# Kernel optimization log

Hardware: AMD Instinct MI355X
Metric: run time of the kernel (lower is better)

## Reference

```python
import jax, jax.numpy as jnp
import numpy as np

DEPTH, DIM, DFF, VOCAB = 4, 512, 2048, 4096
EPS = 1e-5

def layernorm(x, w, b):
    mu = jnp.mean(x, axis=-1, keepdims=True)
    var = jnp.mean((x - mu) ** 2, axis=-1, keepdims=True)
    return (x - mu) * jax.lax.rsqrt(var + EPS) * w + b

def sconv(x, phazor_c, last_conv_c):
    # x: [B,L,dim] real; phazor_c, last_conv_c: [dim] complex
    B, L, D = x.shape
    r = jnp.abs(phazor_c)
    p = jnp.tanh(r) * jnp.exp(1j * jnp.angle(phazor_c))          # [dim]
    prog = p[None, :] ** jnp.arange(L, dtype=jnp.float32)[:, None]  # [L,dim]
    filt_fft = jnp.fft.fft(prog, n=2 * L, axis=0)                # [2L,dim]
    x_fft = jnp.fft.fft(x.astype(jnp.complex64), n=2 * L, axis=1)  # [B,2L,dim]
    conv = jnp.fft.ifft(filt_fft[None] * x_fft, axis=1)[:, :L]   # [B,L,dim]
    conv = conv + last_conv_c[None, None, :] * prog[None] * p[None, None, :]
    return conv.real.astype(x.dtype)

def setup_inputs() -> dict:
    key = jax.random.key(0)
    ks = jax.random.split(key, 20)
    f32 = jnp.float32
    inp = {}
    inp['x'] = jax.random.normal(ks[0], (2, 4096, VOCAB), dtype=f32)
    inp['Win'] = jax.random.normal(ks[1], (DIM, VOCAB), dtype=f32) * VOCAB ** -0.5
    inp['bin'] = jnp.zeros((DIM,), f32)
    inp['ln1_w'] = jnp.ones((DEPTH, DIM), f32)
    inp['ln1_b'] = jnp.zeros((DEPTH, DIM), f32)
    # phazor init: exp(2*pi*i*arange/dim)*|randn|
    ang = 2 * np.pi * jnp.arange(DIM, dtype=f32) / DIM
    mag = jnp.abs(jax.random.normal(ks[2], (DEPTH, DIM), dtype=f32))
    inp['phz_re'] = mag * jnp.cos(ang)[None]
    inp['phz_im'] = mag * jnp.sin(ang)[None]
    inp['lc_re'] = jax.random.normal(ks[3], (DEPTH, DIM), dtype=f32)
    inp['lc_im'] = jax.random.normal(ks[4], (DEPTH, DIM), dtype=f32)
    inp['sc_lin'] = jnp.ones((DEPTH, DIM), f32)
    inp['ln2_w'] = jnp.ones((DEPTH, DIM), f32)
    inp['ln2_b'] = jnp.zeros((DEPTH, DIM), f32)
    inp['W1'] = jax.random.normal(ks[5], (DEPTH, DFF, DIM), dtype=f32) * DIM ** -0.5
    inp['b1'] = jnp.zeros((DEPTH, DFF), f32)
    inp['W2'] = jax.random.normal(ks[6], (DEPTH, DIM, DFF), dtype=f32) * DFF ** -0.5
    inp['b2'] = jnp.zeros((DEPTH, DIM), f32)
    inp['lnl_w'] = jnp.ones((DIM,), f32)
    inp['lnl_b'] = jnp.zeros((DIM,), f32)
    inp['Wout'] = jax.random.normal(ks[7], (VOCAB, DIM), dtype=f32) * DIM ** -0.5
    inp['bout'] = jnp.zeros((VOCAB,), f32)
    return inp

def _forward(x, Win, bin, ln1_w, ln1_b, phz_re, phz_im, lc_re, lc_im, sc_lin,
             ln2_w, ln2_b, W1, b1, W2, b2, lnl_w, lnl_b, Wout, bout):
    h = jnp.einsum('blv,dv->bld', x, Win) + bin  # token_in

    def body(h, p):
        l1w, l1b, pr, pi, lr, li, scl, l2w, l2b, w1, b1_, w2, b2_ = p
        y = jax.nn.silu(layernorm(h, l1w, l1b))
        y = sconv(y, pr + 1j * pi, lr + 1j * li)
        h = h + y * scl
        y = layernorm(h, l2w, l2b)
        y = jax.nn.silu(jnp.einsum('bld,fd->blf', y, w1) + b1_)
        y = jnp.einsum('blf,df->bld', y, w2) + b2_
        return h + y, None

    xs = (ln1_w, ln1_b, phz_re, phz_im, lc_re, lc_im, sc_lin,
          ln2_w, ln2_b, W1, b1, W2, b2)
    h, _ = jax.lax.scan(body, h, xs)
    h = layernorm(h, lnl_w, lnl_b)
    return jnp.einsum('bld,vd->blv', h, Wout) + bout

def reference(x, Win, bin, ln1_w, ln1_b, phz_re, phz_im, lc_re, lc_im, sc_lin,
              ln2_w, ln2_b, W1, b1, W2, b2, lnl_w, lnl_b, Wout, bout):
    return _forward(x, Win, bin, ln1_w, ln1_b, phz_re, phz_im, lc_re, lc_im,
                    sc_lin, ln2_w, ln2_b, W1, b1, W2, b2, lnl_w, lnl_b, Wout, bout)
```

## Files before the change

### kernel.cpp

```cpp
#include <hip/hip_runtime.h>
#include <hip/hip_bf16.h>
#include <cstdint>
#include <cstddef>

#define DEPTH 4
#define DIM 512
#define DFF 2048
#define VOCAB 4096
#define NB 2
#define LSEQ 4096
#define MR (NB*LSEQ)
#define EPSL 1e-5f
#define NC 256
#define TCH 16

typedef __attribute__((ext_vector_type(8))) short  s8v;
typedef __attribute__((ext_vector_type(4))) float  f4v;
typedef __attribute__((ext_vector_type(8))) __bf16 bf8v;

__device__ __forceinline__ unsigned short f2b(float f) {
  union { float f; unsigned int u; } v; v.f = f;
  unsigned int r = v.u + 0x7FFFu + ((v.u >> 16) & 1u);
  return (unsigned short)(r >> 16);
}
__device__ __forceinline__ float b2f(unsigned short u) {
  union { unsigned int u; float f; } v; v.u = ((unsigned int)u) << 16; return v.f;
}

__device__ __forceinline__ void gld16(const void* g, void* l) {
  __builtin_amdgcn_global_load_lds(
      (const __attribute__((address_space(1))) unsigned int*)(uintptr_t)g,
      (__attribute__((address_space(3))) unsigned int*)(uintptr_t)l,
      16, 0, 0);
}

template<int N> __device__ __forceinline__ void wvm() {
  if constexpr (N == 8)      asm volatile("s_waitcnt vmcnt(8)" ::: "memory");
  else if constexpr (N == 6) asm volatile("s_waitcnt vmcnt(6)" ::: "memory");
  else if constexpr (N == 4) asm volatile("s_waitcnt vmcnt(4)" ::: "memory");
  else if constexpr (N == 3) asm volatile("s_waitcnt vmcnt(3)" ::: "memory");
  else                       asm volatile("s_waitcnt vmcnt(0)" ::: "memory");
}

__device__ __forceinline__ void wred64(float& s, float& s2) {
#pragma unroll
  for (int off = 32; off; off >>= 1) { s += __shfl_xor(s, off, 64); s2 += __shfl_xor(s2, off, 64); }
}

#define NX8 4194304
#define NW8  262144
#define N18  524288
#define N28  524288
#define NO8  262144
__global__ void __launch_bounds__(256) cvt_all(
    const float* __restrict__ x,  const float* __restrict__ Win,
    const float* __restrict__ W1, const float* __restrict__ W2,
    const float* __restrict__ Wout,
    unsigned short* __restrict__ xb,  unsigned short* __restrict__ Winb,
    unsigned short* __restrict__ W1b, unsigned short* __restrict__ W2b,
    unsigned short* __restrict__ Woutb)
{
  long i = (long)blockIdx.x * 256 + threadIdx.x;
  const float* src; unsigned short* dst; long j;
  if (i < NX8)                         { src = x;    dst = xb;    j = i; }
  else if (i < NX8 + NW8)              { src = Win;  dst = Winb;  j = i - NX8; }
  else if (i < NX8 + NW8 + N18)        { src = W1;   dst = W1b;   j = i - NX8 - NW8; }
  else if (i < NX8 + NW8 + N18 + N28)  { src = W2;   dst = W2b;   j = i - NX8 - NW8 - N18; }
  else                                 { src = Wout; dst = Woutb; j = i - NX8 - NW8 - N18 - N28; }
  const f4v* p = (const f4v*)(src + j * 8);
  f4v a = p[0], b = p[1];
  s8v o;
  o[0]=(short)f2b(a[0]); o[1]=(short)f2b(a[1]); o[2]=(short)f2b(a[2]); o[3]=(short)f2b(a[3]);
  o[4]=(short)f2b(b[0]); o[5]=(short)f2b(b[1]); o[6]=(short)f2b(b[2]); o[7]=(short)f2b(b[3]);
  *(s8v*)(dst + j * 8) = o;
}

__device__ __forceinline__ void phz2p(float re, float im, float& pre, float& pim) {
  float r = sqrtf(re * re + im * im);
  float t = (r > 1e-20f) ? (tanhf(r) / r) : 1.0f;
  pre = t * re; pim = t * im;
}

__device__ __forceinline__ void ln_silu_emit(
    float (*ls)[DIM], unsigned short* __restrict__ y,
    const float* __restrict__ lnw, const float* __restrict__ lnb,
    int wave, int c8, int b, int c)
{
  f4v w0 = *(const f4v*)(lnw + c8), w1 = *(const f4v*)(lnw + c8 + 4);
  f4v b0 = *(const f4v*)(lnb + c8), b1 = *(const f4v*)(lnb + c8 + 4);
#pragma unroll
  for (int jj = 0; jj < 2; ++jj) {
    int j = wave * 2 + jj;
    f4v v0 = *(const f4v*)&ls[j][c8];
    f4v v1 = *(const f4v*)&ls[j][c8 + 4];
    float s = 0.f, s2 = 0.f;
#pragma unroll
    for (int q = 0; q < 4; ++q) { s += v0[q]; s2 += v0[q]*v0[q]; s += v1[q]; s2 += v1[q]*v1[q]; }
    wred64(s, s2);
    float mu = s * (1.f / DIM);
    float rs = rsqrtf(s2 * (1.f / DIM) - mu * mu + EPSL);
    s8v ob;
    f4v o0, o1;
#pragma unroll
    for (int q = 0; q < 4; ++q) {
      float a = (v0[q] - mu) * rs * w0[q] + b0[q];
      a = a / (1.f + __expf(-a));
      unsigned short ua = f2b(a);
      ob[q] = (short)ua; o0[q] = b2f(ua);
      float e = (v1[q] - mu) * rs * w1[q] + b1[q];
      e = e / (1.f + __expf(-e));
      unsigned short ue = f2b(e);
      ob[4 + q] = (short)ue; o1[q] = b2f(ue);
    }
    *(s8v*)(y + ((size_t)b * LSEQ + (size_t)c * TCH + j) * DIM + c8) = ob;
    *(f4v*)&ls[j][c8]     = o0;
    *(f4v*)&ls[j][c8 + 4] = o1;
  }
}

__global__ void __launch_bounds__(512) red_ln_scan(
    const float* __restrict__ parts, float* __restrict__ h, const float* __restrict__ bias,
    const float* __restrict__ lnw, const float* __restrict__ lnb,
    const float* __restrict__ pr, const float* __restrict__ pi,
    unsigned short* __restrict__ y, float* __restrict__ stA)
{
  __shared__ float ls[TCH][DIM];
  const int d = threadIdx.x;
  const int c = blockIdx.x, b = blockIdx.y;
  const size_t rbase = ((size_t)b * LSEQ + (size_t)c * TCH) * DIM + d;
  const size_t st = (size_t)MR * DIM;
  const float bv = bias[d];
#pragma unroll 4
  for (int j = 0; j < TCH; ++j) {
    size_t o = rbase + (size_t)j * DIM;
    float v = parts[o] + parts[st + o] + bv;
    h[o] = v;
    ls[j][d] = v;
  }
  __syncthreads();
  const int wave = threadIdx.x >> 6, lane = threadIdx.x & 63;
  ln_silu_emit(ls, y, lnw, lnb, wave, lane * 8, b, c);
  __syncthreads();
  float pre, pim; phz2p(pr[d], pi[d], pre, pim);
  float sre = 0.f, sim = 0.f;
#pragma unroll
  for (int j = 0; j < TCH; ++j) {
    float xv = ls[j][d];
    float nre = fmaf(pre, sre, fmaf(-pim, sim, xv));
    float nim = fmaf(pre, sim, pim * sre);
    sre = nre; sim = nim;
  }
  size_t o = (((size_t)b * NC + c) * DIM + d) * 2;
  stA[o] = sre; stA[o + 1] = sim;
}

__global__ void __launch_bounds__(512) ln_scan(
    const float* __restrict__ h,
    const float* __restrict__ lnw, const float* __restrict__ lnb,
    const float* __restrict__ pr, const float* __restrict__ pi,
    unsigned short* __restrict__ y, float* __restrict__ stA)
{
  __shared__ float ls[TCH][DIM];
  const int d = threadIdx.x;
  const int c = blockIdx.x, b = blockIdx.y;
  const size_t rbase = ((size_t)b * LSEQ + (size_t)c * TCH) * DIM + d;
#pragma unroll 4
  for (int j = 0; j < TCH; ++j) ls[j][d] = h[rbase + (size_t)j * DIM];
  __syncthreads();
  const int wave = threadIdx.x >> 6, lane = threadIdx.x & 63;
  ln_silu_emit(ls, y, lnw, lnb, wave, lane * 8, b, c);
  __syncthreads();
  float pre, pim; phz2p(pr[d], pi[d], pre, pim);
  float sre = 0.f, sim = 0.f;
#pragma unroll
  for (int j = 0; j < TCH; ++j) {
    float xv = ls[j][d];
    float nre = fmaf(pre, sre, fmaf(-pim, sim, xv));
    float nim = fmaf(pre, sim, pim * sre);
    sre = nre; sim = nim;
  }
  size_t o = (((size_t)b * NC + c) * DIM + d) * 2;
  stA[o] = sre; stA[o + 1] = sim;
}

__global__ void __launch_bounds__(256) scan_b(
    const float* __restrict__ stA, float* __restrict__ carry,
    const float* __restrict__ pr, const float* __restrict__ pi,
    const float* __restrict__ lcr, const float* __restrict__ lci)
{
  int idx = blockIdx.x * 256 + threadIdx.x;
  int b = idx >> 9, d = idx & (DIM - 1);
  float pre, pim; phz2p(pr[d], pi[d], pre, pim);
  float qre = pre, qim = pim;
#pragma unroll
  for (int t = 0; t < 4; ++t) { float nr = qre*qre - qim*qim; float ni = 2.f*qre*qim; qre = nr; qim = ni; }
  float cre = lcr[d], cim = lci[d];
  const size_t base = (size_t)b * NC * DIM * 2 + (size_t)d * 2;
  for (int c0 = 0; c0 < NC; c0 += 8) {
    float ar[8], ai[8];
#pragma unroll
    for (int k = 0; k < 8; ++k) {
      size_t o = base + (size_t)(c0 + k) * DIM * 2;
      ar[k] = stA[o]; ai[k] = stA[o + 1];
    }
#pragma unroll
    for (int k = 0; k < 8; ++k) {
      size_t o = base + (size_t)(c0 + k) * DIM * 2;
      carry[o] = cre; carry[o + 1] = cim;
      float nr = fmaf(qre, cre, fmaf(-qim, cim, ar[k]));
      float ni = fmaf(qre, cim, fmaf(qim, cre, ai[k]));
      cre = nr; cim = ni;
    }
  }
}

__global__ void __launch_bounds__(512) scan_c_ln2(
    const unsigned short* __restrict__ y, float* __restrict__ h, const float* __restrict__ carry,
    const float* __restrict__ pr, const float* __restrict__ pi,
    const float* __restrict__ scl,
    const float* __restrict__ lnw, const float* __restrict__ lnb,
    unsigned short* __restrict__ yb)
{
  __shared__ float ls[TCH][DIM];
  const int d = threadIdx.x;
  const int c = blockIdx.x, b = blockIdx.y;
  float pre, pim; phz2p(pr[d], pi[d], pre, pim);
  size_t co = (((size_t)b * NC + c) * DIM + d) * 2;
  float sre = carry[co], sim = carry[co + 1];
  const float sc = scl[d];
  const size_t rbase = ((size_t)b * LSEQ + (size_t)c * TCH) * DIM + d;
#pragma unroll 4
  for (int j = 0; j < TCH; ++j) {
    size_t o = rbase + (size_t)j * DIM;
    float xv = b2f(y[o]);
    float nre = fmaf(pre, sre, fmaf(-pim, sim, xv));
    float nim = fmaf(pre, sim, pim * sre);
    sre = nre; sim = nim;
    float hv = h[o] + sre * sc;
    h[o] = hv;
    ls[j][d] = hv;
  }
  __syncthreads();
  const int wave = threadIdx.x >> 6, lane = threadIdx.x & 63;
  const int c8 = lane * 8;
  f4v w0 = *(const f4v*)(lnw + c8), w1 = *(const f4v*)(lnw + c8 + 4);
  f4v b0 = *(const f4v*)(lnb + c8), b1 = *(const f4v*)(lnb + c8 + 4);
#pragma unroll
  for (int jj = 0; jj < 2; ++jj) {
    int j = wave * 2 + jj;
    f4v v0 = *(const f4v*)&ls[j][c8];
    f4v v1 = *(const f4v*)&ls[j][c8 + 4];
    float s = 0.f, s2 = 0.f;
#pragma unroll
    for (int q = 0; q < 4; ++q) { s += v0[q]; s2 += v0[q]*v0[q]; s += v1[q]; s2 += v1[q]*v1[q]; }
    wred64(s, s2);
    float mu = s * (1.f / DIM);
    float rs = rsqrtf(s2 * (1.f / DIM) - mu * mu + EPSL);
    s8v o;
#pragma unroll
    for (int q = 0; q < 4; ++q) {
      o[q]     = (short)f2b((v0[q] - mu) * rs * w0[q] + b0[q]);
      o[4 + q] = (short)f2b((v1[q] - mu) * rs * w1[q] + b1[q]);
    }
    *(s8v*)(yb + ((size_t)b * LSEQ + (size_t)c * TCH + j) * DIM + c8) = o;
  }
}

__global__ void __launch_bounds__(512) ln_final(
    const float* __restrict__ h,
    const float* __restrict__ lnw, const float* __restrict__ lnb,
    unsigned short* __restrict__ yb)
{
  __shared__ float ls[TCH][DIM];
  const int d = threadIdx.x;
  const int c = blockIdx.x, b = blockIdx.y;
  const size_t rbase = ((size_t)b * LSEQ + (size_t)c * TCH) * DIM + d;
#pragma unroll 4
  for (int j = 0; j < TCH; ++j) ls[j][d] = h[rbase + (size_t)j * DIM];
  __syncthreads();
  const int wave = threadIdx.x >> 6, lane = threadIdx.x & 63;
  const int c8 = lane * 8;
  f4v w0 = *(const f4v*)(lnw + c8), w1 = *(const f4v*)(lnw + c8 + 4);
  f4v b0 = *(const f4v*)(lnb + c8), b1 = *(const f4v*)(lnb + c8 + 4);
#pragma unroll
  for (int jj = 0; jj < 2; ++jj) {
    int j = wave * 2 + jj;
    f4v v0 = *(const f4v*)&ls[j][c8];
    f4v v1 = *(const f4v*)&ls[j][c8 + 4];
    float s = 0.f, s2 = 0.f;
#pragma unroll
    for (int q = 0; q < 4; ++q) { s += v0[q]; s2 += v0[q]*v0[q]; s += v1[q]; s2 += v1[q]*v1[q]; }
    wred64(s, s2);
    float mu = s * (1.f / DIM);
    float rs = rsqrtf(s2 * (1.f / DIM) - mu * mu + EPSL);
    s8v o;
#pragma unroll
    for (int q = 0; q < 4; ++q) {
      o[q]     = (short)f2b((v0[q] - mu) * rs * w0[q] + b0[q]);
      o[4 + q] = (short)f2b((v1[q] - mu) * rs * w1[q] + b1[q]);
    }
    *(s8v*)(yb + ((size_t)b * LSEQ + (size_t)c * TCH + j) * DIM + c8) = o;
  }
}

template<int EPI, int BN>
__global__ void __launch_bounds__(256, BN == 64 ? 4 : 3) gemm_p(
    const unsigned short* __restrict__ A, const unsigned short* __restrict__ Bm,
    const float* __restrict__ bias,
    float* __restrict__ Cf, unsigned short* __restrict__ Cb,
    int N, int Keff, int lda, int ldb)
{
  constexpr int WN  = BN / 2;
  constexpr int NJ  = WN / 16;
  constexpr int VPT = 2 + BN / 64;
  __shared__ unsigned short As[3][128 * 32];
  __shared__ unsigned short Bs[3][BN * 32];
  const int tid  = threadIdx.x;
  const int lane = tid & 63, wave = tid >> 6;
  const int wm = wave >> 1, wn = wave & 1;
  const int fr = lane & 15, fq = lane >> 4;
  const int bz = blockIdx.z;

  int bx, by;
  {
    int gx = gridDim.x;
    int nwg = gx * gridDim.y;
    int b = blockIdx.y * gx + blockIdx.x;
    int lid = (b & 7) * (nwg >> 3) + (b >> 3);
    bx = lid % gx; by = lid / gx;
  }
  const int m0 = by * 128, n0 = bx * BN;
  const int koff = bz * Keff;
  const int nkt = Keff >> 5;

  f4v acc[4][NJ];
#pragma unroll
  for (int i = 0; i < 4; ++i)
#pragma unroll
    for (int j = 0; j < NJ; ++j) acc[i][j] = (f4v){0.f, 0.f, 0.f, 0.f};

  const int row2 = tid >> 2, col2 = (tid & 3) << 3;
  auto stage = [&](int buf, int kt) {
    const unsigned short* Ab = A  + (size_t)m0 * lda + koff + kt * 32;
    const unsigned short* Bb = Bm + (size_t)n0 * ldb + koff + kt * 32;
    gld16(Ab + (size_t)row2 * lda + col2,        &As[buf][tid * 8]);
    gld16(Ab + (size_t)(row2 + 64) * lda + col2, &As[buf][(256 + tid) * 8]);
    gld16(Bb + (size_t)row2 * ldb + col2,        &Bs[buf][tid * 8]);
    if constexpr (BN == 128)
      gld16(Bb + (size_t)(row2 + 64) * ldb + col2, &Bs[buf][(256 + tid) * 8]);
  };

  stage(0, 0);
  stage(1, 1);

  int b0 = 0, b1 = 1, b2 = 2;
  for (int kt = 0; kt < nkt; ++kt) {
    bool pf = (kt + 2 < nkt);
    if (pf) stage(b2, kt + 2);
    if (pf)                    wvm<2 * VPT>();
    else if (kt + 1 < nkt)     wvm<VPT>();
    else                       wvm<0>();
    __builtin_amdgcn_s_barrier();
    __builtin_amdgcn_sched_barrier(0);
    bf8v av[4], bv[NJ];
#pragma unroll
    for (int i = 0; i < 4; ++i)
      av[i] = *(const bf8v*)&As[b0][(wm * 64 + i * 16 + fr) * 32 + fq * 8];
#pragma unroll
    for (int j = 0; j < NJ; ++j)
      bv[j] = *(const bf8v*)&Bs[b0][(wn * WN + j * 16 + fr) * 32 + fq * 8];
#pragma unroll
    for (int i = 0; i < 4; ++i)
#pragma unroll
      for (int j = 0; j < NJ; ++j)
        acc[i][j] = __builtin_amdgcn_mfma_f32_16x16x32_bf16(av[i], bv[j], acc[i][j], 0, 0, 0);
    __builtin_amdgcn_sched_barrier(0);
    __builtin_amdgcn_s_barrier();
    int t = b0; b0 = b1; b1 = b2; b2 = t;
  }

  const size_t pbase = (EPI == 3) ? (size_t)bz * MR * N : 0;
#pragma unroll
  for (int j = 0; j < NJ; ++j) {
    const int col = n0 + wn * WN + j * 16 + fr;
    const float bsv = (EPI == 3) ? 0.f : bias[col];
#pragma unroll
    for (int i = 0; i < 4; ++i) {
#pragma unroll
      for (int r = 0; r < 4; ++r) {
        const int row = m0 + wm * 64 + i * 16 + fq * 4 + r;
        const size_t off = (size_t)row * N + col;
        float v = acc[i][j][r] + bsv;
        if constexpr (EPI == 0) {
          Cf[off] = v;
        } else if constexpr (EPI == 1) {
          float sv = v / (1.f + __expf(-v));
          Cb[off] = f2b(sv);
        } else if constexpr (EPI == 2) {
          Cf[off] = Cf[off] + v;
        } else {
          Cf[pbase + off] = v;
        }
      }
    }
  }
}

extern "C" void kernel_launch(void* const* d_in, const int* in_sizes, int n_in,
                              void* d_out, int out_size, void* d_ws, size_t ws_size,
                              hipStream_t stream)
{
  (void)in_sizes; (void)n_in; (void)out_size; (void)ws_size;
  const float* x    = (const float*)d_in[0];
  const float* Win  = (const float*)d_in[1];
  const float* bin  = (const float*)d_in[2];
  const float* ln1w = (const float*)d_in[3];
  const float* ln1b = (const float*)d_in[4];
  const float* phzr = (const float*)d_in[5];
  const float* phzi = (const float*)d_in[6];
  const float* lcr  = (const float*)d_in[7];
  const float* lci  = (const float*)d_in[8];
  const float* scl  = (const float*)d_in[9];
  const float* ln2w = (const float*)d_in[10];
  const float* ln2b = (const float*)d_in[11];
  const float* W1   = (const float*)d_in[12];
  const float* b1   = (const float*)d_in[13];
  const float* W2   = (const float*)d_in[14];
  const float* b2   = (const float*)d_in[15];
  const float* lnlw = (const float*)d_in[16];
  const float* lnlb = (const float*)d_in[17];
  const float* Wout = (const float*)d_in[18];
  const float* bout = (const float*)d_in[19];

  char* wsp = (char*)d_ws;
  auto alloc = [&](size_t bytes) { char* p = wsp; wsp += (bytes + 255) & ~(size_t)255; return p; };
  float*          h     = (float*)alloc((size_t)MR * DIM * 4);
  unsigned short* y     = (unsigned short*)alloc((size_t)MR * DIM * 2);
  unsigned short* yb    = (unsigned short*)alloc((size_t)MR * DIM * 2);
  unsigned short* Winb  = (unsigned short*)alloc((size_t)DIM * VOCAB * 2);
  unsigned short* W1b   = (unsigned short*)alloc((size_t)DEPTH * DFF * DIM * 2);
  unsigned short* W2b   = (unsigned short*)alloc((size_t)DEPTH * DIM * DFF * 2);
  unsigned short* Woutb = (unsigned short*)alloc((size_t)VOCAB * DIM * 2);
  float*          stA   = (float*)alloc((size_t)NB * NC * DIM * 2 * 4);
  float*          carry = (float*)alloc((size_t)NB * NC * DIM * 2 * 4);

  unsigned short* xb    = (unsigned short*)d_out;
  unsigned short* act1  = (unsigned short*)d_out;
  float*          parts = (float*)((char*)d_out + ((size_t)64 << 20));

  dim3 blk(256);
  dim3 fblk(512);
  dim3 fgrid(NC, NB);
  cvt_all<<<dim3((NX8 + NW8 + N18 + N28 + NO8) / 256), blk, 0, stream>>>(
      x, Win, W1, W2, Wout, xb, Winb, W1b, W2b, Woutb);

  gemm_p<3, 128><<<dim3(DIM / 128, MR / 128, 2), blk, 0, stream>>>(
      xb, Winb, nullptr, parts, nullptr, DIM, VOCAB / 2, VOCAB, VOCAB);
  red_ln_scan<<<fgrid, fblk, 0, stream>>>(parts, h, bin, ln1w, ln1b, phzr, phzi, y, stA);

  for (int l = 0; l < DEPTH; ++l) {
    scan_b<<<dim3((NB * DIM) / 256), blk, 0, stream>>>(stA, carry, phzr + l * DIM, phzi + l * DIM,
                                                       lcr + l * DIM, lci + l * DIM);
    scan_c_ln2<<<fgrid, fblk, 0, stream>>>(y, h, carry, phzr + l * DIM, phzi + l * DIM,
                                           scl + l * DIM, ln2w + l * DIM, ln2b + l * DIM, yb);
    gemm_p<1, 128><<<dim3(DFF / 128, MR / 128, 1), blk, 0, stream>>>(
        yb, W1b + (size_t)l * DFF * DIM, b1 + l * DFF, nullptr, act1, DFF, DIM, DIM, DIM);
    gemm_p<2, 64><<<dim3(DIM / 64, MR / 128, 1), blk, 0, stream>>>(
        act1, W2b + (size_t)l * DIM * DFF, b2 + l * DIM, h, nullptr, DIM, DFF, DFF, DFF);
    if (l < DEPTH - 1) {
      ln_scan<<<fgrid, fblk, 0, stream>>>(h, ln1w + (l + 1) * DIM, ln1b + (l + 1) * DIM,
                                          phzr + (l + 1) * DIM, phzi + (l + 1) * DIM, y, stA);
    }
  }
  ln_final<<<fgrid, fblk, 0, stream>>>(h, lnlw, lnlb, yb);
  gemm_p<0, 128><<<dim3(VOCAB / 128, MR / 128, 1), blk, 0, stream>>>(
      yb, Woutb, bout, (float*)d_out, nullptr, VOCAB, DIM, DIM, DIM);
}
```

Before: 565.4 us.

## Fuse fp32-to-bf16 conversion of input into token-embedding GEMM A-tile loads

Removes the separate pass that converted the large fp32 input activation to bf16. A new GEMM kernel instead streams fp32 A tiles into LDS with an XOR swizzle and converts them to bf16 in registers before the MFMA. This is meant to cut the extra write and read of the converted input. The cost is a larger LDS footprint per block (lower occupancy) and twice as many global bytes per A tile inside the GEMM.

```diff
diff --git a/kernel.cpp b/kernel.cpp
--- a/kernel.cpp
+++ b/kernel.cpp
@@ -35,7 +35,8 @@
 }
 
 template<int N> __device__ __forceinline__ void wvm() {
-  if constexpr (N == 8)      asm volatile("s_waitcnt vmcnt(8)" ::: "memory");
+  if constexpr (N == 12)     asm volatile("s_waitcnt vmcnt(12)" ::: "memory");
+  else if constexpr (N == 8) asm volatile("s_waitcnt vmcnt(8)" ::: "memory");
   else if constexpr (N == 6) asm volatile("s_waitcnt vmcnt(6)" ::: "memory");
   else if constexpr (N == 4) asm volatile("s_waitcnt vmcnt(4)" ::: "memory");
   else if constexpr (N == 3) asm volatile("s_waitcnt vmcnt(3)" ::: "memory");
@@ -47,26 +48,24 @@
   for (int off = 32; off; off >>= 1) { s += __shfl_xor(s, off, 64); s2 += __shfl_xor(s2, off, 64); }
 }
 
-#define NX8 4194304
 #define NW8  262144
 #define N18  524288
 #define N28  524288
 #define NO8  262144
 __global__ void __launch_bounds__(256) cvt_all(
-    const float* __restrict__ x,  const float* __restrict__ Win,
+    const float* __restrict__ Win,
     const float* __restrict__ W1, const float* __restrict__ W2,
     const float* __restrict__ Wout,
-    unsigned short* __restrict__ xb,  unsigned short* __restrict__ Winb,
+    unsigned short* __restrict__ Winb,
     unsigned short* __restrict__ W1b, unsigned short* __restrict__ W2b,
     unsigned short* __restrict__ Woutb)
 {
   long i = (long)blockIdx.x * 256 + threadIdx.x;
   const float* src; unsigned short* dst; long j;
-  if (i < NX8)                         { src = x;    dst = xb;    j = i; }
-  else if (i < NX8 + NW8)              { src = Win;  dst = Winb;  j = i - NX8; }
-  else if (i < NX8 + NW8 + N18)        { src = W1;   dst = W1b;   j = i - NX8 - NW8; }
-  else if (i < NX8 + NW8 + N18 + N28)  { src = W2;   dst = W2b;   j = i - NX8 - NW8 - N18; }
-  else                                 { src = Wout; dst = Woutb; j = i - NX8 - NW8 - N18 - N28; }
+  if (i < NW8)                   { src = Win;  dst = Winb;  j = i; }
+  else if (i < NW8 + N18)        { src = W1;   dst = W1b;   j = i - NW8; }
+  else if (i < NW8 + N18 + N28)  { src = W2;   dst = W2b;   j = i - NW8 - N18; }
+  else                           { src = Wout; dst = Woutb; j = i - NW8 - N18 - N28; }
   const f4v* p = (const f4v*)(src + j * 8);
   f4v a = p[0], b = p[1];
   s8v o;
@@ -319,7 +318,6 @@
   const int lane = tid & 63, wave = tid >> 6;
   const int wm = wave >> 1, wn = wave & 1;
   const int fr = lane & 15, fq = lane >> 4;
-  const int bz = blockIdx.z;
 
   int bx, by;
   {
@@ -330,7 +328,6 @@
     bx = lid % gx; by = lid / gx;
   }
   const int m0 = by * 128, n0 = bx * BN;
-  const int koff = bz * Keff;
   const int nkt = Keff >> 5;
 
   f4v acc[4][NJ];
@@ -341,8 +338,8 @@
 
   const int row2 = tid >> 2, col2 = (tid & 3) << 3;
   auto stage = [&](int buf, int kt) {
-    const unsigned short* Ab = A  + (size_t)m0 * lda + koff + kt * 32;
-    const unsigned short* Bb = Bm + (size_t)n0 * ldb + koff + kt * 32;
+    const unsigned short* Ab = A  + (size_t)m0 * lda + kt * 32;
+    const unsigned short* Bb = Bm + (size_t)n0 * ldb + kt * 32;
     gld16(Ab + (size_t)row2 * lda + col2,        &As[buf][tid * 8]);
     gld16(Ab + (size_t)(row2 + 64) * lda + col2, &As[buf][(256 + tid) * 8]);
     gld16(Bb + (size_t)row2 * ldb + col2,        &Bs[buf][tid * 8]);
@@ -379,11 +376,10 @@
     int t = b0; b0 = b1; b1 = b2; b2 = t;
   }
 
-  const size_t pbase = (EPI == 3) ? (size_t)bz * MR * N : 0;
 #pragma unroll
   for (int j = 0; j < NJ; ++j) {
     const int col = n0 + wn * WN + j * 16 + fr;
-    const float bsv = (EPI == 3) ? 0.f : bias[col];
+    const float bsv = bias[col];
 #pragma unroll
     for (int i = 0; i < 4; ++i) {
 #pragma unroll
@@ -396,11 +392,105 @@
         } else if constexpr (EPI == 1) {
           float sv = v / (1.f + __expf(-v));
           Cb[off] = f2b(sv);
-        } else if constexpr (EPI == 2) {
+        } else {
           Cf[off] = Cf[off] + v;
-        } else {
-          Cf[pbase + off] = v;
         }
+      }
+    }
+  }
+}
+
+__global__ void __launch_bounds__(256, 2) gemm_tokf(
+    const float* __restrict__ A, const unsigned short* __restrict__ Bm,
+    float* __restrict__ Cf, int N, int Keff, int lda, int ldb)
+{
+  __shared__ float          Asf[3][128 * 32];
+  __shared__ unsigned short Bs[3][128 * 32];
+  const int tid  = threadIdx.x;
+  const int lane = tid & 63, wave = tid >> 6;
+  const int wm = wave >> 1, wn = wave & 1;
+  const int fr = lane & 15, fq = lane >> 4;
+  const int bz = blockIdx.z;
+
+  int bx, by;
+  {
+    int gx = gridDim.x;
+    int nwg = gx * gridDim.y;
+    int b = blockIdx.y * gx + blockIdx.x;
+    int lid = (b & 7) * (nwg >> 3) + (b >> 3);
+    bx = lid % gx; by = lid / gx;
+  }
+  const int m0 = by * 128, n0 = bx * 128;
+  const int koff = bz * Keff;
+  const int nkt = Keff >> 5;
+
+  f4v acc[4][4];
+#pragma unroll
+  for (int i = 0; i < 4; ++i)
+#pragma unroll
+    for (int j = 0; j < 4; ++j) acc[i][j] = (f4v){0.f, 0.f, 0.f, 0.f};
+
+  const int row2 = tid >> 2, col2 = (tid & 3) << 3;
+  auto stage = [&](int buf, int kt) {
+    const float* Ab = A + (size_t)m0 * lda + koff + kt * 32;
+    const unsigned short* Bb = Bm + (size_t)n0 * ldb + koff + kt * 32;
+#pragma unroll
+    for (int q = 0; q < 4; ++q) {
+      int s = q * 256 + tid;
+      int row = s >> 3;
+      int c4  = (s & 7) ^ (row & 7);
+      gld16(Ab + (size_t)row * lda + c4 * 4, &Asf[buf][s * 4]);
+    }
+    gld16(Bb + (size_t)row2 * ldb + col2,        &Bs[buf][tid * 8]);
+    gld16(Bb + (size_t)(row2 + 64) * ldb + col2, &Bs[buf][(256 + tid) * 8]);
+  };
+
+  stage(0, 0);
+  stage(1, 1);
+
+  int b0 = 0, b1 = 1, b2 = 2;
+  for (int kt = 0; kt < nkt; ++kt) {
+    bool pf = (kt + 2 < nkt);
+    if (pf) stage(b2, kt + 2);
+    if (pf)                    wvm<12>();
+    else if (kt + 1 < nkt)     wvm<6>();
+    else                       wvm<0>();
+    __builtin_amdgcn_s_barrier();
+    __builtin_amdgcn_sched_barrier(0);
+    bf8v av[4], bv[4];
+#pragma unroll
+    for (int i = 0; i < 4; ++i) {
+      int arow = wm * 64 + i * 16 + fr;
+      int g0 = arow * 8 + ((fq * 2) ^ (arow & 7));
+      int g1 = g0 ^ 1;
+      f4v lo = *(const f4v*)&Asf[b0][g0 * 4];
+      f4v hi = *(const f4v*)&Asf[b0][g1 * 4];
+#pragma unroll
+      for (int q = 0; q < 4; ++q) { av[i][q] = (__bf16)lo[q]; av[i][4 + q] = (__bf16)hi[q]; }
+    }
+#pragma unroll
+    for (int j = 0; j < 4; ++j)
+      bv[j] = *(const bf8v*)&Bs[b0][(wn * 64 + j * 16 + fr) * 32 + fq * 8];
+#pragma unroll
+    for (int i = 0; i < 4; ++i)
+#pragma unroll
+      for (int j = 0; j < 4; ++j)
+        acc[i][j] = __builtin_amdgcn_mfma_f32_16x16x32_bf16(av[i], bv[j], acc[i][j], 0, 0, 0);
+    __builtin_amdgcn_sched_barrier(0);
+    __builtin_amdgcn_s_barrier();
+    int t = b0; b0 = b1; b1 = b2; b2 = t;
+  }
+
+  const size_t pbase = (size_t)bz * MR * N;
+#pragma unroll
+  for (int j = 0; j < 4; ++j) {
+    const int col = n0 + wn * 64 + j * 16 + fr;
+#pragma unroll
+    for (int i = 0; i < 4; ++i) {
+#pragma unroll
+      for (int r = 0; r < 4; ++r) {
+        const int row = m0 + wm * 64 + i * 16 + fq * 4 + r;
+        Cf[pbase + (size_t)row * N + col] = acc[i][j][r];
       }
     }
   }
@@ -444,18 +534,17 @@
   float*          stA   = (float*)alloc((size_t)NB * NC * DIM * 2 * 4);
   float*          carry = (float*)alloc((size_t)NB * NC * DIM * 2 * 4);
 
-  unsigned short* xb    = (unsigned short*)d_out;
   unsigned short* act1  = (unsigned short*)d_out;
   float*          parts = (float*)((char*)d_out + ((size_t)64 << 20));
 
   dim3 blk(256);
   dim3 fblk(512);
   dim3 fgrid(NC, NB);
-  cvt_all<<<dim3((NX8 + NW8 + N18 + N28 + NO8) / 256), blk, 0, stream>>>(
-      x, Win, W1, W2, Wout, xb, Winb, W1b, W2b, Woutb);
-
-  gemm_p<3, 128><<<dim3(DIM / 128, MR / 128, 2), blk, 0, stream>>>(
-      xb, Winb, nullptr, parts, nullptr, DIM, VOCAB / 2, VOCAB, VOCAB);
+  cvt_all<<<dim3((NW8 + N18 + N28 + NO8) / 256), blk, 0, stream>>>(
+      Win, W1, W2, Wout, Winb, W1b, W2b, Woutb);
+
+  gemm_tokf<<<dim3(DIM / 128, MR / 128, 2), blk, 0, stream>>>(
+      x, Winb, parts, DIM, VOCAB / 2, VOCAB, VOCAB);
   red_ln_scan<<<fgrid, fblk, 0, stream>>>(parts, h, bin, ln1w, ln1b, phzr, phzi, y, stA);
 
   for (int l = 0; l < DEPTH; ++l) {
@@ -463,9 +552,9 @@
                                                        lcr + l * DIM, lci + l * DIM);
     scan_c_ln2<<<fgrid, fblk, 0, stream>>>(y, h, carry, phzr + l * DIM, phzi + l * DIM,
                                            scl + l * DIM, ln2w + l * DIM, ln2b + l * DIM, yb);
-    gemm_p<1, 128><<<dim3(DFF / 128, MR / 128, 1), blk, 0, stream>>>(
+    gemm_p<1, 128><<<dim3(DFF / 128, MR / 128), blk, 0, stream>>>(
         yb, W1b + (size_t)l * DFF * DIM, b1 + l * DFF, nullptr, act1, DFF, DIM, DIM, DIM);
-    gemm_p<2, 64><<<dim3(DIM / 64, MR / 128, 1), blk, 0, stream>>>(
+    gemm_p<2, 64><<<dim3(DIM / 64, MR / 128), blk, 0, stream>>>(
         act1, W2b + (size_t)l * DIM * DFF, b2 + l * DIM, h, nullptr, DIM, DFF, DFF, DFF);
     if (l < DEPTH - 1) {
       ln_scan<<<fgrid, fblk, 0, stream>>>(h, ln1w + (l + 1) * DIM, ln1b + (l + 1) * DIM,
@@ -473,6 +562,6 @@
     }
   }
   ln_final<<<fgrid, fblk, 0, stream>>>(h, lnlw, lnlb, yb);
-  gemm_p<0, 128><<<dim3(VOCAB / 128, MR / 128, 1), blk, 0, stream>>>(
+  gemm_p<0, 128><<<dim3(VOCAB / 128, MR / 128), blk, 0, stream>>>(
       yb, Woutb, bout, (float*)d_out, nullptr, VOCAB, DIM, DIM, DIM);
 }
```

Measured after the change: 572.0 us. Within noise of the previous version (+1.2%).
